# Kernel optimization log

Hardware: AMD Instinct MI355X
Metric: run time of the kernel (lower is better)

The kernel has to match this reference:

```python
import jax, jax.numpy as jnp
import numpy as np

S, B, H, V = 64, 8, 512, 8192  # seq_length, batch, hidden, vocab
NEG = -1e9  # finite stand-in for -inf so gradients stay clean


def setup_inputs() -> dict:
    key = jax.random.key(0)
    ks = jax.random.split(key, 8)
    lin = lambda k, fi, fo: jax.random.normal(k, (fi, fo), jnp.float32) * 0.05
    return dict(
        h=jax.random.normal(ks[0], (S, B, H), jnp.float32) * 0.1,
        sentence=jax.random.randint(ks[1], (S, B), 0, V),
        t_W1=lin(ks[2], 2 * H, H), t_b1=jnp.zeros((H,), jnp.float32),
        t_W2=lin(ks[3], H, 1), t_b2=jnp.zeros((1,), jnp.float32),
        w_W1=lin(ks[4], 2 * H, H), w_b1=jnp.zeros((H,), jnp.float32),
        w_W2=lin(ks[5], H, V), w_b2=jnp.zeros((V,), jnp.float32),
    )


def _inside(h, sentence, t_W1, t_b1, t_W2, t_b2, w_W1, w_b1, w_W2, w_b2):
    sent_length = S - 1
    # ---- transition scores on full (i, j) grid: concat(h_i, h_j) -> MLP -> scalar
    hi = jnp.broadcast_to(h[:, None], (S, S, B, H))
    hj = jnp.broadcast_to(h[None, :], (S, S, B, H))
    feat = jnp.concatenate([hi, hj], axis=-1)                      # [S,S,B,2H]
    t = (jax.nn.relu(feat @ t_W1 + t_b1) @ t_W2 + t_b2)[..., 0]    # [S,S,B]
    sh_lp = jax.nn.log_sigmoid(-t)   # log p(shift | i, j)
    re_lp = jax.nn.log_sigmoid(t)    # log p(reduce | i, j)

    # ---- word generation log-probs for pairs (i, j), i < j <= sent_length-1
    iu, ju = jnp.triu_indices(sent_length, k=1)                    # P pairs
    hp = jnp.concatenate([h[iu], h[ju]], axis=-1)                  # [P,B,2H]
    logits = jax.nn.relu(hp @ w_W1 + w_b1) @ w_W2 + w_b2           # [P,B,V]
    lse = jax.scipy.special.logsumexp(logits, axis=-1)             # [P,B]
    tok = sentence[ju + 1]                                         # [P,B]
    tok_logit = jnp.take_along_axis(logits, tok[..., None], axis=-1)[..., 0]
    word_lp = tok_logit - lse
    # shift prob + word prob (word_prob_list in the original)
    wp = jnp.full((S, S, B), NEG, jnp.float32).at[iu, ju].set(sh_lp[iu, ju] + word_lp)

    # ---- DP table init
    table = jnp.full((S, S, B), NEG, jnp.float32)
    f0 = jnp.concatenate([h[0], h[0]], axis=-1)                    # [B,2H]
    lg0 = jax.nn.relu(f0 @ w_W1 + w_b1) @ w_W2 + w_b2              # [B,V]
    init_lp = jnp.take_along_axis(jax.nn.log_softmax(lg0, axis=-1),
                                  sentence[1][:, None], axis=1)[:, 0]
    table = table.at[0, 1].set(init_lp)
    jd = jnp.arange(1, sent_length)
    table = table.at[jd, jd + 1].set(0.0)

    # ---- diagonal sweep: table[i,j] = LSE_k( table[i,k]+table[k,j]+wp[i,k]+re[k,j] )
    ivec = jnp.arange(S)
    mvec = jnp.arange(1, S)

    def step(tab, g):
        i = ivec[:, None]
        m = mvec[None, :]
        k = jnp.clip(i + m, 0, S - 1)                              # [S,S-1]
        jv = jnp.clip(ivec + g, 0, S - 1)                          # [S]
        j = jv[:, None]
        valid = (m < g) & (ivec[:, None] + g <= sent_length)       # [S,S-1]
        sc = tab[i, k] + tab[k, j] + wp[i, k] + re_lp[k, j]        # [S,S-1,B]
        sc = jnp.where(valid[..., None], sc, NEG)
        mmax = jnp.max(sc, axis=1, keepdims=True)
        new = jnp.log(jnp.sum(jnp.exp(sc - mmax), axis=1)) + mmax[:, 0]
        row_ok = (ivec + g <= sent_length)[:, None]
        tab = tab.at[ivec, jv].set(jnp.where(row_ok, new, tab[ivec, jv]))
        return tab, None

    table, _ = jax.lax.scan(step, table, jnp.arange(2, sent_length + 1))
    final = table[0, sent_length] + re_lp[0, sent_length]          # [B]
    return -jnp.sum(final)  # neg_log_likelihood


def reference(h, sentence, t_W1, t_b1, t_W2, t_b2, w_W1, w_b1, w_W2, w_b2):
    return _inside(h, sentence, t_W1, t_b1, t_W2, t_b2, w_W1, w_b1, w_W2, w_b2)
```

## Files before the change

### kernel.cpp

```cpp
#include <hip/hip_runtime.h>
#include <hip/hip_bf16.h>
#include <hip/hip_fp8.h>
#include <math.h>

#define NEG (-1.0e9f)

typedef __bf16 bf16_t;
typedef __bf16 bf16x4 __attribute__((ext_vector_type(4)));
typedef __bf16 bf16x8 __attribute__((ext_vector_type(8)));
typedef float f32x4 __attribute__((ext_vector_type(4)));
typedef float f32x16 __attribute__((ext_vector_type(16)));
typedef int i32x4 __attribute__((ext_vector_type(4)));
typedef int i32x8 __attribute__((ext_vector_type(8)));
typedef unsigned char u8;
typedef unsigned long long u64;

#define SS 64
#define BB 8
#define HH 512
#define VV 8192
#define NPAIR 1953
#define NPTOT 1954
#define MROWS (NPTOT*BB)
#define MPAD  16384

__device__ __forceinline__ float logsig(float x) {
  return fminf(x, 0.f) - __logf(1.f + __expf(-fabsf(x)));
}
__device__ __forceinline__ u8 f2q(float x) { __hip_fp8_e4m3 q(x); return q.__x; }
__device__ __forceinline__ float q2f(u8 b) { __hip_fp8_e4m3 q; q.__x = b; return (float)q; }

__global__ __launch_bounds__(256) void k_prep(
    const float* __restrict__ h,   bf16_t* __restrict__ hbf,
    const float* __restrict__ tW1, bf16_t* __restrict__ tW1T,
    const float* __restrict__ wW1, bf16_t* __restrict__ wW1T,
    const float* __restrict__ wW2, u8* __restrict__ w2t8) {
  __shared__ float tile[32][33];
  int blk = blockIdx.x, tid = threadIdx.x;
  if (blk < 256) {
    int gi = blk * 256 + tid;
    float4 v = ((const float4*)h)[gi];
    bf16x4 o = {(bf16_t)v.x, (bf16_t)v.y, (bf16_t)v.z, (bf16_t)v.w};
    ((bf16x4*)hbf)[gi] = o;
    return;
  }
  if (blk < 1280) {
    const float* in; bf16_t* out; int R = 1024, C = 512, t;
    if (blk < 768) { in = tW1; out = tW1T; t = blk - 256; }
    else           { in = wW1; out = wW1T; t = blk - 768; }
    int xt = C / 32;
    int c0 = (t % xt) * 32, r0 = (t / xt) * 32;
    int tx = tid & 31, ty = tid >> 5;
    for (int i = ty; i < 32; i += 8)
      tile[i][tx] = in[(size_t)(r0 + i) * C + c0 + tx];
    __syncthreads();
    for (int i = ty; i < 32; i += 8)
      out[(size_t)(c0 + i) * R + r0 + tx] = (bf16_t)tile[tx][i];
    return;
  }
  int t = blk - 1280;
  int c0 = (t % 256) * 32, r0 = (t / 256) * 32;
  int tx = tid & 31, ty = tid >> 5;
  for (int i = ty; i < 32; i += 8)
    tile[i][tx] = wW2[(size_t)(r0 + i) * 8192 + c0 + tx];
  __syncthreads();
  for (int i = ty; i < 32; i += 8)
    w2t8[(size_t)(c0 + i) * 512 + r0 + tx] = f2q(tile[tx][i]);
}

__global__ __launch_bounds__(256) void k_gemm4(
    const bf16_t* __restrict__ A,
    const bf16_t* __restrict__ tW1T, const bf16_t* __restrict__ wW1T,
    float* __restrict__ Ut, float* __restrict__ Vt,
    float* __restrict__ Uw, float* __restrict__ Vw)
{
  __shared__ __align__(16) bf16_t As[128 * 32];
  __shared__ __align__(16) bf16_t Bs[128 * 32];
  const int tid = threadIdx.x;
  const int lane = tid & 63;
  const int wave = tid >> 6;
  const int wr = wave >> 1, wc = wave & 1;
  const int sel = blockIdx.x >> 4, sub = blockIdx.x & 15;
  const bf16_t* BT = (sel < 2 ? tW1T : wW1T) + (sel & 1) * 512;
  float* Cout = (sel == 0) ? Ut : (sel == 1) ? Vt : (sel == 2) ? Uw : Vw;
  const int m0 = (sub & 3) * 128, n0 = (sub >> 2) * 128;
  const int lda = 512, ldb = 1024, ldc = 512;

  const int rowS = tid >> 2;
  const int kS = (tid & 3) * 8;
  const bf16_t* gA0 = A + (size_t)(m0 + rowS) * lda + kS;
  const bf16_t* gA1 = A + (size_t)(m0 + rowS + 64) * lda + kS;
  const bf16_t* gB0 = BT + (size_t)(n0 + rowS) * ldb + kS;
  const bf16_t* gB1 = BT + (size_t)(n0 + rowS + 64) * ldb + kS;

  f32x4 acc[4][4] = {};
  const int aoff = (wr * 64 + (lane & 15)) * 32 + (lane >> 4) * 8;
  const int boff = (wc * 64 + (lane & 15)) * 32 + (lane >> 4) * 8;

  for (int k0 = 0; k0 < 512; k0 += 32) {
    __builtin_amdgcn_global_load_lds((const __attribute__((address_space(1))) void*)(gA0 + k0),
        (__attribute__((address_space(3))) void*)(As + wave * 512), 16, 0, 0);
    __builtin_amdgcn_global_load_lds((const __attribute__((address_space(1))) void*)(gA1 + k0),
        (__attribute__((address_space(3))) void*)(As + 2048 + wave * 512), 16, 0, 0);
    __builtin_amdgcn_global_load_lds((const __attribute__((address_space(1))) void*)(gB0 + k0),
        (__attribute__((address_space(3))) void*)(Bs + wave * 512), 16, 0, 0);
    __builtin_amdgcn_global_load_lds((const __attribute__((address_space(1))) void*)(gB1 + k0),
        (__attribute__((address_space(3))) void*)(Bs + 2048 + wave * 512), 16, 0, 0);
    __syncthreads();
    bf16x8 af[4], bfr[4];
    #pragma unroll
    for (int mf = 0; mf < 4; ++mf) af[mf] = *(const bf16x8*)&As[aoff + mf * 16 * 32];
    #pragma unroll
    for (int nf = 0; nf < 4; ++nf) bfr[nf] = *(const bf16x8*)&Bs[boff + nf * 16 * 32];
    #pragma unroll
    for (int mf = 0; mf < 4; ++mf)
      #pragma unroll
      for (int nf = 0; nf < 4; ++nf)
        acc[mf][nf] = __builtin_amdgcn_mfma_f32_16x16x32_bf16(af[mf], bfr[nf], acc[mf][nf], 0, 0, 0);
    __syncthreads();
  }
  #pragma unroll
  for (int mf = 0; mf < 4; ++mf)
    #pragma unroll
    for (int r2 = 0; r2 < 4; ++r2) {
      int grow = m0 + wr * 64 + mf * 16 + (lane >> 4) * 4 + r2;
      #pragma unroll
      for (int nf = 0; nf < 4; ++nf) {
        int gcol = n0 + wc * 64 + nf * 16 + (lane & 15);
        Cout[(size_t)grow * ldc + gcol] = acc[mf][nf][r2];
      }
    }
}

#define STAGEA(b, h, kt) do { \
  const u8* _s = A8 + (size_t)(m0 + (h)*128 + (tid>>2)) * 512 + (kt)*64 + csrc; \
  __builtin_amdgcn_global_load_lds((const __attribute__((address_space(1))) void*)_s, \
    (__attribute__((address_space(3))) void*)(As + (b)*16384 + (h)*8192 + (tid>>6)*1024), 16, 0, 0); \
} while(0)

#define STAGEB(b, h, kt) do { \
  const u8* _s = BT8 + (size_t)(n0 + (h)*128 + (tid>>2)) * 512 + (kt)*64 + csrc; \
  __builtin_amdgcn_global_load_lds((const __attribute__((address_space(1))) void*)_s, \
    (__attribute__((address_space(3))) void*)(Bs + (b)*16384 + (h)*8192 + (tid>>6)*1024), 16, 0, 0); \
} while(0)

#define LDA(b, mh) do { \
  i32x4 _l0 = *(const i32x4*)(As + (b)*16384 + (mh)*8192 + aoff0); \
  i32x4 _h0 = *(const i32x4*)(As + (b)*16384 + (mh)*8192 + aoff1); \
  aF0 = __builtin_shufflevector(_l0, _h0, 0,1,2,3,4,5,6,7); \
  i32x4 _l1 = *(const i32x4*)(As + (b)*16384 + (mh)*8192 + aoff0 + 2048); \
  i32x4 _h1 = *(const i32x4*)(As + (b)*16384 + (mh)*8192 + aoff1 + 2048); \
  aF1 = __builtin_shufflevector(_l1, _h1, 0,1,2,3,4,5,6,7); \
} while(0)

#define LDB(b, nh) do { \
  i32x4 _l = *(const i32x4*)(Bs + (b)*16384 + (nh)*8192 + boff0); \
  i32x4 _h = *(const i32x4*)(Bs + (b)*16384 + (nh)*8192 + boff1); \
  bF = __builtin_shufflevector(_l, _h, 0,1,2,3,4,5,6,7); \
} while(0)

#define ACC(mh, ms, nh) acc[(mh)*4 + (ms)*2 + (nh)]

#define MMA(mh, nh) do { \
  __builtin_amdgcn_s_setprio(1); \
  ACC(mh,0,nh) = __builtin_amdgcn_mfma_scale_f32_32x32x64_f8f6f4( \
      aF0, bF, ACC(mh,0,nh), 0, 0, 0, 0x7F7F7F7F, 0, 0x7F7F7F7F); \
  ACC(mh,1,nh) = __builtin_amdgcn_mfma_scale_f32_32x32x64_f8f6f4( \
      aF1, bF, ACC(mh,1,nh), 0, 0, 0, 0x7F7F7F7F, 0, 0x7F7F7F7F); \
  __builtin_amdgcn_s_setprio(0); \
} while(0)

#define BARLG() do { __builtin_amdgcn_s_barrier(); \
  asm volatile("s_waitcnt lgkmcnt(0)" ::: "memory"); \
  __builtin_amdgcn_sched_barrier(0); } while(0)
#define ENDPH() __builtin_amdgcn_s_barrier()
#define CKPT() asm volatile("s_waitcnt vmcnt(2)" ::: "memory")

__global__ __launch_bounds__(512, 2) void k_gemm256(
    const u8* __restrict__ A8,
    const u8* __restrict__ BT8,
    const float* __restrict__ bias,
    float* __restrict__ sumexp)
{
  __shared__ __align__(16) u8 As[2 * 16384];
  __shared__ __align__(16) u8 Bs[2 * 16384];
  const int tid = threadIdx.x;
  const int l = tid & 63;
  const int wave = tid >> 6;
  const int wr = wave >> 2, wc = wave & 3;

  const int xcd = blockIdx.x & 7, sub = blockIdx.x >> 3;
  const int mt = xcd * 8 + (sub & 7);
  const int nt = sub >> 3;
  const int m0 = mt * 256, n0 = nt * 256;

  const int csrc = (((tid & 3) ^ ((tid >> 3) & 3)) << 4);
  const int u0 = (l >> 5) * 2;
  const int rA = wr * 64 + (l & 31);
  const int sA = (rA >> 1) & 3;
  const int aoff0 = rA * 64 + ((u0 ^ sA) << 4);
  const int aoff1 = rA * 64 + (((u0 + 1) ^ sA) << 4);
  const int rB = wc * 32 + (l & 31);
  const int sB = (rB >> 1) & 3;
  const int boff0 = rB * 64 + ((u0 ^ sB) << 4);
  const int boff1 = rB * 64 + (((u0 + 1) ^ sB) << 4);

  f32x16 acc[8] = {};
  i32x8 aF0, aF1, bF;

  STAGEA(0, 0, 0); STAGEA(0, 1, 0); STAGEB(0, 0, 0); STAGEB(0, 1, 0);
  STAGEA(1, 0, 1); STAGEB(1, 0, 1);
  CKPT();
  __builtin_amdgcn_s_barrier();

  #pragma unroll 1
  for (int t = 0; t < 4; ++t) {
    int tA = 2 * t + 1;
    int tB = 2 * t + 2; if (tB > 7) tB = 7;
    int tC = 2 * t + 3; if (tC > 7) tC = 7;
    LDA(0, 0); LDB(0, 0); STAGEA(1, 1, tA); BARLG(); MMA(0, 0); ENDPH();
    LDB(0, 1);            STAGEB(1, 1, tA); BARLG(); MMA(0, 1); ENDPH();
    LDA(0, 1); LDB(0, 0); STAGEA(0, 0, tB); BARLG(); MMA(1, 0); ENDPH();
    LDB(0, 1);            STAGEB(0, 0, tB); BARLG(); MMA(1, 1); CKPT(); ENDPH();
    LDA(1, 0); LDB(1, 0); STAGEA(0, 1, tB); BARLG(); MMA(0, 0); ENDPH();
    LDB(1, 1);            STAGEB(0, 1, tB); BARLG(); MMA(0, 1); ENDPH();
    LDA(1, 1); LDB(1, 0); STAGEA(1, 0, tC); BARLG(); MMA(1, 0); ENDPH();
    LDB(1, 1);            STAGEB(1, 0, tC); BARLG(); MMA(1, 1); CKPT(); ENDPH();
  }

  float b2v0 = bias[n0 + wc * 32 + (l & 31)];
  float b2v1 = bias[n0 + 128 + wc * 32 + (l & 31)];
  const int hf = (l >> 5) * 4;
  #pragma unroll
  for (int mh = 0; mh < 2; ++mh) {
    #pragma unroll
    for (int ms = 0; ms < 2; ++ms) {
      f32x16 A0 = ACC(mh, ms, 0), A1 = ACC(mh, ms, 1);
      #pragma unroll
      for (int rg = 0; rg < 16; ++rg) {
        float s = __expf(A0[rg] + b2v0) + __expf(A1[rg] + b2v1);
        s += __shfl_xor(s, 1); s += __shfl_xor(s, 2);
        s += __shfl_xor(s, 4); s += __shfl_xor(s, 8);
        s += __shfl_xor(s, 16);
        if ((l & 31) == 0)
          atomicAdd(&sumexp[m0 + mh * 128 + wr * 64 + ms * 32 + (rg & 3) + 8 * (rg >> 2) + hf], s);
      }
    }
  }
}

__global__ __launch_bounds__(256) void k_act(const float* __restrict__ Uw, const float* __restrict__ Vw,
                                             const float* __restrict__ b1, u8* __restrict__ act8,
                                             float* __restrict__ sumexp,
                                             const u8* __restrict__ w2t8, const int* __restrict__ sent,
                                             const float* __restrict__ b2, float* __restrict__ tok_logit) {
  __shared__ float pd[512];
  int p = blockIdx.x;
  if (threadIdx.x < 8) sumexp[p * 8 + threadIdx.x] = 0.f;
  int iu = 0, ju = 0;
  bool real = (p < NPTOT);
  if (p < NPAIR) {
    int i = 0, base = 0;
    while (base + (62 - i) <= p) { base += 62 - i; ++i; }
    iu = i; ju = i + 1 + (p - base);
  }
  const int srow = (p < NPAIR) ? (ju + 1) : 1;
  for (int t = threadIdx.x; t < 512; t += 256) {
    int b = t >> 6, c = t & 63;
    u64 bytes = 0;
    if (real) {
      const float4* u4 = (const float4*)(Uw + (size_t)(iu * BB + b) * HH);
      const float4* v4 = (const float4*)(Vw + (size_t)(ju * BB + b) * HH);
      const float4* bb4 = (const float4*)b1;
      #pragma unroll
      for (int q = 0; q < 2; ++q) {
        float4 uu = u4[c * 2 + q], vv = v4[c * 2 + q], bb = bb4[c * 2 + q];
        bytes |= (u64)f2q(fmaxf(uu.x + vv.x + bb.x, 0.f)) << (8 * (q * 4 + 0));
        bytes |= (u64)f2q(fmaxf(uu.y + vv.y + bb.y, 0.f)) << (8 * (q * 4 + 1));
        bytes |= (u64)f2q(fmaxf(uu.z + vv.z + bb.z, 0.f)) << (8 * (q * 4 + 2));
        bytes |= (u64)f2q(fmaxf(uu.w + vv.w + bb.w, 0.f)) << (8 * (q * 4 + 3));
      }
    }
    *(u64*)(act8 + (size_t)(p * 8 + b) * 512 + c * 8) = bytes;
    float s = 0.f;
    if (real) {
      int tok = sent[srow * BB + b];
      u64 wv = *(const u64*)(w2t8 + (size_t)tok * 512 + c * 8);
      #pragma unroll
      for (int e = 0; e < 8; ++e)
        s += q2f((u8)(bytes >> (8 * e))) * q2f((u8)(wv >> (8 * e)));
    }
    pd[t] = s;
  }
  __syncthreads();
  if (real) {
    int wv_ = threadIdx.x >> 6, ln = threadIdx.x & 63;
    #pragma unroll
    for (int rr = 0; rr < 2; ++rr) {
      int b = wv_ * 2 + rr;
      float s = pd[b * 64 + ln];
      #pragma unroll
      for (int off = 1; off < 64; off <<= 1) s += __shfl_xor(s, off);
      if (ln == 0) {
        int tok = sent[srow * BB + b];
        tok_logit[p * 8 + b] = s + b2[tok];
      }
    }
  }
}

__global__ __launch_bounds__(256) void k_tnet(const float* __restrict__ Ut, const float* __restrict__ Vt,
                                              const float* __restrict__ b1, const float* __restrict__ W2,
                                              const float* __restrict__ b2,
                                              float* __restrict__ sh_lp, float* __restrict__ re_lp) {
  int gid = blockIdx.x * 4 + (threadIdx.x >> 6);
  int lane = threadIdx.x & 63;
  int b = gid & 7, j = (gid >> 3) & 63, i = gid >> 9;
  const float4* u = (const float4*)(Ut + (size_t)(i * BB + b) * HH);
  const float4* v = (const float4*)(Vt + (size_t)(j * BB + b) * HH);
  const float4* bb = (const float4*)b1;
  const float4* ww = (const float4*)W2;
  float s = 0.f;
  #pragma unroll
  for (int qq = 0; qq < 2; ++qq) {
    int c = lane * 2 + qq;
    float4 uu = u[c], vv = v[c], b4 = bb[c], w4 = ww[c];
    s += fmaxf(uu.x + vv.x + b4.x, 0.f) * w4.x;
    s += fmaxf(uu.y + vv.y + b4.y, 0.f) * w4.y;
    s += fmaxf(uu.z + vv.z + b4.z, 0.f) * w4.z;
    s += fmaxf(uu.w + vv.w + b4.w, 0.f) * w4.w;
  }
  #pragma unroll
  for (int off = 1; off < 64; off <<= 1) s += __shfl_xor(s, off);
  if (lane == 0) {
    float t = s + b2[0];
    re_lp[gid] = logsig(t);
    sh_lp[gid] = logsig(-t);
  }
}

__global__ __launch_bounds__(1024) void k_dp(const float* __restrict__ sh_lp, const float* __restrict__ re_lp,
                                             const float* __restrict__ tok_logit, const float* __restrict__ sumexp,
                                             float* __restrict__ finals) {
  int b = blockIdx.x;
  __shared__ float tab[4096];
  __shared__ float wpl[4096];
  __shared__ float rel[4096];
  int tid = threadIdx.x;
  for (int idx = tid; idx < 4096; idx += 1024) {
    tab[idx] = NEG;
    int i = idx >> 6, j = idx & 63;
    float w = NEG;
    if (i < j && j <= 62) {
      int p = i * 62 - i * (i - 1) / 2 + (j - i - 1);
      int r = p * 8 + b;
      w = sh_lp[idx * 8 + b] + (tok_logit[r] - __logf(sumexp[r]));
    }
    wpl[idx] = w;
    rel[idx] = re_lp[idx * 8 + b];
  }
  __syncthreads();
  if (tid == 0) tab[1] = tok_logit[NPAIR * 8 + b] - __logf(sumexp[NPAIR * 8 + b]);
  if (tid >= 1 && tid <= 62) tab[tid * 64 + tid + 1] = 0.f;
  __syncthreads();
  int lane = tid & 63, wave = tid >> 6;
  for (int g = 2; g <= 63; ++g) {
    int cnt = 64 - g;
    if (g <= 17) {
      int seg = lane >> 4, sl = lane & 15;
      int i = wave * 4 + seg;
      if (i < cnt) {
        int m = sl + 1;
        int j = i + g, k = i + m;
        float sc = NEG;
        if (m < g) sc = tab[i * 64 + k] + tab[k * 64 + j] + wpl[i * 64 + k] + rel[k * 64 + j];
        float mx = sc;
        #pragma unroll
        for (int off = 1; off < 16; off <<= 1) mx = fmaxf(mx, __shfl_xor(mx, off));
        float e = (m < g) ? __expf(sc - mx) : 0.f;
        #pragma unroll
        for (int off = 1; off < 16; off <<= 1) e += __shfl_xor(e, off);
        if (sl == 0) tab[i * 64 + j] = __logf(e) + mx;
      }
    } else {
      for (int i = wave; i < cnt; i += 16) {
        int m = lane + 1;
        int j = i + g, k = i + m;
        float sc = NEG;
        if (m < g) sc = tab[i * 64 + k] + tab[k * 64 + j] + wpl[i * 64 + k] + rel[k * 64 + j];
        float mx = sc;
        #pragma unroll
        for (int off = 1; off < 64; off <<= 1) mx = fmaxf(mx, __shfl_xor(mx, off));
        float e = (m < g) ? __expf(sc - mx) : 0.f;
        #pragma unroll
        for (int off = 1; off < 64; off <<= 1) e += __shfl_xor(e, off);
        if (lane == 0) tab[i * 64 + j] = __logf(e) + mx;
      }
    }
    __syncthreads();
  }
  if (tid == 0) finals[b] = tab[63] + rel[63];
}

__global__ void k_final(const float* __restrict__ finals, float* __restrict__ out) {
  if (threadIdx.x == 0) {
    float s = 0.f;
    for (int b = 0; b < 8; ++b) s += finals[b];
    out[0] = -s;
  }
}

extern "C" void kernel_launch(void* const* d_in, const int* in_sizes, int n_in,
                              void* d_out, int out_size, void* d_ws, size_t ws_size,
                              hipStream_t stream) {
  const float* h    = (const float*)d_in[0];
  const int*   sent = (const int*)d_in[1];
  const float* tW1  = (const float*)d_in[2];
  const float* tb1  = (const float*)d_in[3];
  const float* tW2  = (const float*)d_in[4];
  const float* tb2  = (const float*)d_in[5];
  const float* wW1  = (const float*)d_in[6];
  const float* wb1  = (const float*)d_in[7];
  const float* wW2  = (const float*)d_in[8];
  const float* wb2  = (const float*)d_in[9];
  float* out = (float*)d_out;

  char* ws = (char*)d_ws;
  size_t off = 0;
  auto alloc = [&](size_t bytes) { char* p = ws + off; off += (bytes + 255) & ~(size_t)255; return p; };
  bf16_t* hbf    = (bf16_t*)alloc((size_t)512 * 512 * 2);
  bf16_t* tW1T   = (bf16_t*)alloc((size_t)512 * 1024 * 2);
  bf16_t* wW1T   = (bf16_t*)alloc((size_t)512 * 1024 * 2);
  u8*     w2t8   = (u8*)alloc((size_t)VV * HH);
  float*  Ut     = (float*)alloc((size_t)512 * 512 * 4);
  float*  Vt     = (float*)alloc((size_t)512 * 512 * 4);
  float*  Uw     = (float*)alloc((size_t)512 * 512 * 4);
  float*  Vw     = (float*)alloc((size_t)512 * 512 * 4);
  u8*     act8   = (u8*)alloc((size_t)MPAD * HH);
  float*  sumexp = (float*)alloc((size_t)MPAD * 4);
  float*  tokl   = (float*)alloc((size_t)MPAD * 4);
  float*  shlp   = (float*)alloc((size_t)32768 * 4);
  float*  relp   = (float*)alloc((size_t)32768 * 4);
  float*  finals = (float*)alloc(256);

  k_prep<<<5376, 256, 0, stream>>>(h, hbf, tW1, tW1T, wW1, wW1T, wW2, w2t8);
  k_gemm4<<<64, 256, 0, stream>>>(hbf, tW1T, wW1T, Ut, Vt, Uw, Vw);
  k_act<<<MPAD / 8, 256, 0, stream>>>(Uw, Vw, wb1, act8, sumexp, w2t8, sent, wb2, tokl);
  k_tnet<<<32768 / 4, 256, 0, stream>>>(Ut, Vt, tb1, tW2, tb2, shlp, relp);
  k_gemm256<<<2048, 512, 0, stream>>>(act8, w2t8, wb2, sumexp);
  k_dp<<<8, 1024, 0, stream>>>(shlp, relp, tokl, sumexp, finals);
  k_final<<<1, 64, 0, stream>>>(finals, out);
}
```

Baseline: 322.4 us.

## Reorganize FP8 GEMM LDS layout and keep both B fragments in registers

Changes the global-to-LDS staging address mapping so each wave's MFMA fragment rows sit in contiguous 1KB chunks, replacing the XOR swizzle with a simple lane-based offset for LDS reads. B fragments are now held in two register slots, so the repeated LDB loads in the second half of each k-step are dropped, cutting LDS read traffic. It costs extra VGPRs and depends on the new staging layout matching what the MFMA operands expect.

```diff
diff --git a/kernel.cpp b/kernel.cpp
--- a/kernel.cpp
+++ b/kernel.cpp
@@ -133,40 +133,40 @@
 }
 
 #define STAGEA(b, h, kt) do { \
-  const u8* _s = A8 + (size_t)(m0 + (h)*128 + (tid>>2)) * 512 + (kt)*64 + csrc; \
+  const u8* _s = A8 + (size_t)(m0 + (h)*128 + rsrc) * 512 + (kt)*64 + ksrc; \
   __builtin_amdgcn_global_load_lds((const __attribute__((address_space(1))) void*)_s, \
     (__attribute__((address_space(3))) void*)(As + (b)*16384 + (h)*8192 + (tid>>6)*1024), 16, 0, 0); \
 } while(0)
 
 #define STAGEB(b, h, kt) do { \
-  const u8* _s = BT8 + (size_t)(n0 + (h)*128 + (tid>>2)) * 512 + (kt)*64 + csrc; \
+  const u8* _s = BT8 + (size_t)(n0 + (h)*128 + rsrc) * 512 + (kt)*64 + ksrc; \
   __builtin_amdgcn_global_load_lds((const __attribute__((address_space(1))) void*)_s, \
     (__attribute__((address_space(3))) void*)(Bs + (b)*16384 + (h)*8192 + (tid>>6)*1024), 16, 0, 0); \
 } while(0)
 
 #define LDA(b, mh) do { \
-  i32x4 _l0 = *(const i32x4*)(As + (b)*16384 + (mh)*8192 + aoff0); \
-  i32x4 _h0 = *(const i32x4*)(As + (b)*16384 + (mh)*8192 + aoff1); \
-  aF0 = __builtin_shufflevector(_l0, _h0, 0,1,2,3,4,5,6,7); \
-  i32x4 _l1 = *(const i32x4*)(As + (b)*16384 + (mh)*8192 + aoff0 + 2048); \
-  i32x4 _h1 = *(const i32x4*)(As + (b)*16384 + (mh)*8192 + aoff1 + 2048); \
-  aF1 = __builtin_shufflevector(_l1, _h1, 0,1,2,3,4,5,6,7); \
+  _Pragma("unroll") \
+  for (int _s2 = 0; _s2 < 2; ++_s2) { \
+    i32x4 _lo = *(const i32x4*)(As + (b)*16384 + (mh)*8192 + (wr*2+_s2)*2048 + rb); \
+    i32x4 _hi = *(const i32x4*)(As + (b)*16384 + (mh)*8192 + (wr*2+_s2)*2048 + 1024 + rb); \
+    aF[_s2] = __builtin_shufflevector(_lo, _hi, 0,1,2,3,4,5,6,7); \
+  } \
 } while(0)
 
-#define LDB(b, nh) do { \
-  i32x4 _l = *(const i32x4*)(Bs + (b)*16384 + (nh)*8192 + boff0); \
-  i32x4 _h = *(const i32x4*)(Bs + (b)*16384 + (nh)*8192 + boff1); \
-  bF = __builtin_shufflevector(_l, _h, 0,1,2,3,4,5,6,7); \
+#define LDB(b, nh, q) do { \
+  i32x4 _lo = *(const i32x4*)(Bs + (b)*16384 + (nh)*8192 + wc*2048 + rb); \
+  i32x4 _hi = *(const i32x4*)(Bs + (b)*16384 + (nh)*8192 + wc*2048 + 1024 + rb); \
+  bFq[q] = __builtin_shufflevector(_lo, _hi, 0,1,2,3,4,5,6,7); \
 } while(0)
 
 #define ACC(mh, ms, nh) acc[(mh)*4 + (ms)*2 + (nh)]
 
-#define MMA(mh, nh) do { \
+#define MMA(mh, nh, q) do { \
   __builtin_amdgcn_s_setprio(1); \
   ACC(mh,0,nh) = __builtin_amdgcn_mfma_scale_f32_32x32x64_f8f6f4( \
-      aF0, bF, ACC(mh,0,nh), 0, 0, 0, 0x7F7F7F7F, 0, 0x7F7F7F7F); \
+      aF[0], bFq[q], ACC(mh,0,nh), 0, 0, 0, 0x7F7F7F7F, 0, 0x7F7F7F7F); \
   ACC(mh,1,nh) = __builtin_amdgcn_mfma_scale_f32_32x32x64_f8f6f4( \
-      aF1, bF, ACC(mh,1,nh), 0, 0, 0, 0x7F7F7F7F, 0, 0x7F7F7F7F); \
+      aF[1], bFq[q], ACC(mh,1,nh), 0, 0, 0, 0x7F7F7F7F, 0, 0x7F7F7F7F); \
   __builtin_amdgcn_s_setprio(0); \
 } while(0)
 
@@ -194,19 +194,18 @@
   const int nt = sub >> 3;
   const int m0 = mt * 256, n0 = nt * 256;
 
-  const int csrc = (((tid & 3) ^ ((tid >> 3) & 3)) << 4);
-  const int u0 = (l >> 5) * 2;
-  const int rA = wr * 64 + (l & 31);
-  const int sA = (rA >> 1) & 3;
-  const int aoff0 = rA * 64 + ((u0 ^ sA) << 4);
-  const int aoff1 = rA * 64 + (((u0 + 1) ^ sA) << 4);
-  const int rB = wc * 32 + (l & 31);
-  const int sB = (rB >> 1) & 3;
-  const int boff0 = rB * 64 + ((u0 ^ sB) << 4);
-  const int boff1 = rB * 64 + (((u0 + 1) ^ sB) << 4);
+  const int msv = tid >> 7;
+  const int iv  = (tid >> 6) & 1;
+  const int xv  = (tid >> 2) & 15;
+  const int uv  = tid & 3;
+  const int rsrc = msv * 32 + (uv & 1) * 16 + xv;
+  const int ksrc = (uv >> 1) * 32 + iv * 16;
+
+  const int rb = (l & 15) * 64 + (l >> 4) * 16;
 
   f32x16 acc[8] = {};
-  i32x8 aF0, aF1, bF;
+  i32x8 aF[2];
+  i32x8 bFq[2];
 
   STAGEA(0, 0, 0); STAGEA(0, 1, 0); STAGEB(0, 0, 0); STAGEB(0, 1, 0);
   STAGEA(1, 0, 1); STAGEB(1, 0, 1);
@@ -218,14 +217,14 @@
     int tA = 2 * t + 1;
     int tB = 2 * t + 2; if (tB > 7) tB = 7;
     int tC = 2 * t + 3; if (tC > 7) tC = 7;
-    LDA(0, 0); LDB(0, 0); STAGEA(1, 1, tA); BARLG(); MMA(0, 0); ENDPH();
-    LDB(0, 1);            STAGEB(1, 1, tA); BARLG(); MMA(0, 1); ENDPH();
-    LDA(0, 1); LDB(0, 0); STAGEA(0, 0, tB); BARLG(); MMA(1, 0); ENDPH();
-    LDB(0, 1);            STAGEB(0, 0, tB); BARLG(); MMA(1, 1); CKPT(); ENDPH();
-    LDA(1, 0); LDB(1, 0); STAGEA(0, 1, tB); BARLG(); MMA(0, 0); ENDPH();
-    LDB(1, 1);            STAGEB(0, 1, tB); BARLG(); MMA(0, 1); ENDPH();
-    LDA(1, 1); LDB(1, 0); STAGEA(1, 0, tC); BARLG(); MMA(1, 0); ENDPH();
-    LDB(1, 1);            STAGEB(1, 0, tC); BARLG(); MMA(1, 1); CKPT(); ENDPH();
+    LDA(0, 0); LDB(0, 0, 0); STAGEA(1, 1, tA); BARLG(); MMA(0, 0, 0); ENDPH();
+    LDB(0, 1, 1);            STAGEB(1, 1, tA); BARLG(); MMA(0, 1, 1); ENDPH();
+    LDA(0, 1);               STAGEA(0, 0, tB); BARLG(); MMA(1, 0, 0); ENDPH();
+                             STAGEB(0, 0, tB); BARLG(); MMA(1, 1, 1); CKPT(); ENDPH();
+    LDA(1, 0); LDB(1, 0, 0); STAGEA(0, 1, tB); BARLG(); MMA(0, 0, 0); ENDPH();
+    LDB(1, 1, 1);            STAGEB(0, 1, tB); BARLG(); MMA(0, 1, 1); ENDPH();
+    LDA(1, 1);               STAGEA(1, 0, tC); BARLG(); MMA(1, 0, 0); ENDPH();
+                             STAGEB(1, 0, tC); BARLG(); MMA(1, 1, 1); CKPT(); ENDPH();
   }
 
   float b2v0 = bias[n0 + wc * 32 + (l & 31)];
```

Result: no change. 319.7 us (-0.8%).
